# Optimization experiments

Hardware: AMD Instinct MI355X
Metric: run time of the kernel (lower is better)

## Reference

```python
import jax, jax.numpy as jnp
import numpy as np

B, C, IN_LEN, OUT_LEN, E, TOP_K, N_I = 1, 8192, 512, 512, 8, 2, 16


def setup_inputs() -> dict:
    key = jax.random.key(0)
    ks = jax.random.split(key, 8)
    w = lambda k, shape, sc=0.02: jax.random.normal(k, shape, dtype=jnp.float32) * sc
    return {
        "x": jax.random.normal(ks[0], (B, C, IN_LEN), dtype=jnp.float32),
        "Ins_tk": jax.random.normal(ks[1], (B, N_I, OUT_LEN), dtype=jnp.float32),
        "gate_w": w(ks[2], (IN_LEN, E)),            # Gate: Linear(in_len, E, bias=False)
        "expert_w": w(ks[3], (E, IN_LEN, OUT_LEN)),  # per-expert Linear weight (transposed)
        "expert_b": jnp.zeros((E, OUT_LEN), dtype=jnp.float32),
        "gamma_w": w(ks[4], (E, OUT_LEN)),          # EiLM gamma_generator: Linear(h,1,bias=False)
        "beta_w": w(ks[5], (E, OUT_LEN, OUT_LEN)),  # EiLM beta_generator (transposed)
        "rmod_w": w(ks[6], (OUT_LEN, E)),           # router_modulator: Linear(out_len, E, bias=False)
    }


def reference(x, Ins_tk, gate_w, expert_w, expert_b, gamma_w, beta_w, rmod_w):
    Bx, Cx, L = x.shape
    xf = x.reshape(-1, L)                                   # [N, in_len], N = B*C
    ins = Ins_tk[0]                                         # [N_i, out_len] (B==1 asserted)

    # Router: logits + expert-wise modulation of logits
    router_gamma = jnp.mean(ins @ rmod_w, axis=0)           # [E]
    logits = xf @ gate_w + router_gamma                     # [N, E]
    probs = jax.nn.softmax(logits.astype(jnp.float32), axis=-1)
    rw, sel = jax.lax.top_k(probs, TOP_K)                   # [N, k] values/indices (no renorm)

    # Combine weights per token per expert: sum_k rw[t,k] * onehot(sel[t,k])
    combine = jnp.sum(jax.nn.one_hot(sel, E, dtype=rw.dtype) * rw[..., None], axis=1)  # [N, E]

    # EiLM per-expert affine params: scalar gamma, vector beta (mean over instruction tokens)
    gam = jnp.mean(ins @ gamma_w.T, axis=0)                 # [E]
    bet = jnp.einsum('nh,ehd->ed', ins, beta_w) / N_I       # [E, out_len]

    # Per-expert linear over all tokens, then EiLM modulation
    eo = jnp.einsum('nl,eld->end', xf, expert_w) + expert_b[:, None, :]   # [E, N, out]
    mod = gam[:, None, None] * eo + bet[:, None, :]                        # [E, N, out]

    out = jnp.einsum('ne,end->nd', combine, mod)            # [N, out]
    return out.reshape(Bx, Cx, OUT_LEN)
```

## Files before the change

kernel.cpp:

```cpp
#include <hip/hip_runtime.h>
#include <hip/hip_bf16.h>

#define N_TOK 8192
#define INL   512
#define OUTL  512
#define NE    8
#define NI    16
#define EOFF  (OUTL * INL)

typedef unsigned short ushort_t;
typedef unsigned int   uint_t;
typedef short  short8  __attribute__((ext_vector_type(8)));
typedef float  floatx4 __attribute__((ext_vector_type(4)));

#define WS_CNT    0u
#define WS_GAM    4096u
#define WS_RGAM   4352u
#define WS_SCHED  4608u
#define WS_BET    8192u
#define WS_SELW   32768u
#define WS_WT     163840u
#define WS_LIST   4358144u
#define WS_XBF    6455296u
#define MAXTP     184

__device__ __forceinline__ ushort_t f2bf(float f) {
    uint_t b = __float_as_uint(f);
    return (ushort_t)((b + 0x7FFFu + ((b >> 16) & 1u)) >> 16);
}
__device__ __forceinline__ uint_t pkbf(float a, float b) {
    __hip_bfloat162 h = __float22bfloat162_rn(make_float2(a, b));
    union { __hip_bfloat162 h2; uint_t u; } cv;
    cv.h2 = h;
    return cv.u;
}
__device__ __forceinline__ void dma16(const ushort_t* g, ushort_t* l) {
    __builtin_amdgcn_global_load_lds(
        (const __attribute__((address_space(1))) void*)g,
        (__attribute__((address_space(3))) void*)l,
        16, 0, 0);
}

__global__ __launch_bounds__(256)
void k_prep(const float* __restrict__ x,
            const float* __restrict__ ins,
            const float* __restrict__ expert_w,
            const float* __restrict__ expert_b,
            const float* __restrict__ gamma_w,
            const float* __restrict__ beta_w,
            const float* __restrict__ rmod_w,
            ushort_t* __restrict__ wt,
            ushort_t* __restrict__ xbf,
            float* __restrict__ wsBet,
            float* __restrict__ wsGam, float* __restrict__ wsRgam,
            int* __restrict__ wsCnt) {
    __shared__ __align__(16) char smem[17152];
    int bx = blockIdx.x;
    int tid = threadIdx.x;

    if (bx < 512) {
        float (*tile)[65] = (float(*)[65])smem;
        int e = bx >> 6, rem = bx & 63;
        int lt = (rem >> 3) * 64, dt = (rem & 7) * 64;
        int dIdx = tid & 63, lq = tid >> 6;
        for (int i = 0; i < 16; ++i) {
            int l = lq * 16 + i;
            tile[l][dIdx] = expert_w[(e * INL + lt + l) * OUTL + dt + dIdx];
        }
        __syncthreads();
        int lIdx = tid & 63, dq = tid >> 6;
        for (int i = 0; i < 16; ++i) {
            int d = dq * 16 + i;
            wt[(e * OUTL + dt + d) * INL + lt + lIdx] = f2bf(tile[lIdx][d]);
        }
        return;
    }

    if (bx < 640) {
        float* sS  = (float*)smem;
        float* red = sS + 512;
        float* gamS = red + 256;
        int b2 = bx - 512;
        int e = b2 >> 4, dBase = (b2 & 15) * 32;
        for (int h = tid; h < INL; h += 256) {
            float a = 0.f;
            for (int n = 0; n < NI; ++n) a += ins[n * INL + h];
            sS[h] = a;
        }
        __syncthreads();
        if (tid < 64) {
            float g = 0.f;
            for (int j = 0; j < 8; ++j) g += sS[tid * 8 + j] * gamma_w[e * INL + tid * 8 + j];
            for (int off = 32; off >= 1; off >>= 1) g += __shfl_xor(g, off, 64);
            if (tid == 0) gamS[0] = g * (1.f / NI);
        }
        int doff = tid & 31, hq = tid >> 5;
        float a = 0.f;
        for (int j = 0; j < 64; ++j) {
            int h = hq * 64 + j;
            a += sS[h] * beta_w[(e * INL + h) * OUTL + dBase + doff];
        }
        red[tid] = a;
        __syncthreads();
        if (tid < 32) {
            float t = 0.f;
            for (int k = 0; k < 8; ++k) t += red[k * 32 + tid];
            int d = dBase + tid;
            wsBet[e * OUTL + d] = t * (1.f / NI) + gamS[0] * expert_b[e * OUTL + d];
        }
        return;
    }

    if (bx == 640) {
        if (tid < 64) wsCnt[tid * 16] = 0;
        float* sS = (float*)smem;
        float* pg = sS + 512;
        float* pr = pg + 64;
        for (int h = tid; h < INL; h += 256) {
            float a = 0.f;
            for (int n = 0; n < NI; ++n) a += ins[n * INL + h];
            sS[h] = a;
        }
        __syncthreads();
        if (tid < 64) {
            int e = tid & 7, qq = tid >> 3;
            float g = 0.f, r = 0.f;
            for (int j = 0; j < 64; ++j) {
                int h = qq * 64 + j;
                float sv = sS[h];
                g += sv * gamma_w[e * INL + h];
                r += sv * rmod_w[h * NE + e];
            }
            pg[tid] = g; pr[tid] = r;
        }
        __syncthreads();
        if (tid < NE) {
            float g = 0.f, r = 0.f;
            for (int qq = 0; qq < 8; ++qq) { g += pg[qq * 8 + tid]; r += pr[qq * 8 + tid]; }
            wsGam[tid]  = g * (1.f / NI);
            wsRgam[tid] = r * (1.f / NI);
        }
        return;
    }

    {
        int b2 = bx - 641;
        const float* xp = x + (size_t)b2 * 16384;
        ushort_t* xq = xbf + (size_t)b2 * 16384;
        #pragma unroll
        for (int j = 0; j < 16; ++j) {
            int o = j * 1024 + tid * 4;
            float4 v = *(const float4*)(xp + o);
            uint2 u;
            u.x = pkbf(v.x, v.y);
            u.y = pkbf(v.z, v.w);
            *(uint2*)(xq + o) = u;
        }
    }
}

__global__ __launch_bounds__(256)
void k_route(const float* __restrict__ x,
             const float* __restrict__ gate_w,
             const float* __restrict__ wsGam,
             const float* __restrict__ wsRgam,
             float4* __restrict__ selW,
             int* __restrict__ wsCnt, int* __restrict__ wsList) {
    __shared__ float gateT[NE * INL];
    __shared__ int tokP[16];
    __shared__ int cnt64[64], base64[64], pos[16];

    int tid = threadIdx.x;
    for (int i = 0; i < 16; ++i) {
        int f = tid + 256 * i;
        gateT[(f & 7) * INL + (f >> 3)] = gate_w[f];
    }
    if (tid < 64) cnt64[tid] = 0;
    __syncthreads();

    int w = tid >> 6, lane = tid & 63;
    int tbase = blockIdx.x * 16 + w * 4;

    for (int tt = 0; tt < 4; ++tt) {
        int t = tbase + tt;
        float2 xv[4];
        for (int i = 0; i < 4; ++i)
            xv[i] = *(const float2*)(x + (size_t)t * INL + 2 * lane + 128 * i);

        float acc[NE];
        for (int e = 0; e < NE; ++e) acc[e] = 0.f;
        for (int i = 0; i < 4; ++i) {
            int c = 2 * lane + 128 * i;
            for (int e = 0; e < NE; ++e)
                acc[e] += xv[i].x * gateT[e * INL + c] + xv[i].y * gateT[e * INL + c + 1];
        }
        for (int e = 0; e < NE; ++e) {
            float a = acc[e];
            for (int off = 32; off >= 1; off >>= 1) a += __shfl_xor(a, off, 64);
            acc[e] = a;
        }
        float logit[NE];
        for (int e = 0; e < NE; ++e) logit[e] = acc[e] + wsRgam[e];

        int i0 = 0; float m0 = logit[0];
        for (int e = 1; e < NE; ++e) if (logit[e] > m0) { m0 = logit[e]; i0 = e; }
        int i1 = -1; float m1 = -3.4e38f;
        for (int e = 0; e < NE; ++e) if (e != i0 && logit[e] > m1) { m1 = logit[e]; i1 = e; }

        float S = 0.f;
        for (int e = 0; e < NE; ++e) S += expf(logit[e] - m0);
        float rw0 = 1.0f / S;
        float rw1 = expf(m1 - m0) / S;

        if (lane == 0) {
            selW[t] = make_float4(rw0 * wsGam[i0], rw1 * wsGam[i1], rw0, rw1);
            tokP[w * 4 + tt] = i0 * 8 + i1;
        }
    }
    __syncthreads();

    if (tid < 16) pos[tid] = atomicAdd(&cnt64[tokP[tid]], 1);
    __syncthreads();
    if (tid < 64 && cnt64[tid] > 0)
        base64[tid] = atomicAdd(wsCnt + tid * 16, cnt64[tid]);
    __syncthreads();
    if (tid < 16) {
        int p = tokP[tid];
        wsList[(size_t)p * N_TOK + base64[p] + pos[tid]] = blockIdx.x * 16 + tid;
    }
}

__global__ __launch_bounds__(256)
void k_sched(const int* __restrict__ wsCnt, int* __restrict__ sched) {
    __shared__ int cnt[64], base[64], totS;
    int tid = threadIdx.x;
    if (tid < 64) cnt[tid] = wsCnt[tid * 16];
    __syncthreads();
    if (tid == 0) {
        int run = 0;
        for (int i = 0; i < 64; ++i) {
            base[i] = run;
            run += (cnt[i] + 63) >> 6;
        }
        totS = run;
    }
    __syncthreads();
    if (tid < 64) {
        int c = cnt[tid], ti = (c + 63) >> 6, b = base[tid];
        for (int j = 0; j < ti; ++j)
            sched[b + j] = tid | (j << 6) | (c << 14);
    }
    for (int j = totS + tid; j < MAXTP; j += 256)
        sched[j] = -1;
}

__global__ __launch_bounds__(256, 4)
void k_gemmp(const ushort_t* __restrict__ xbf, const ushort_t* __restrict__ wt,
             const int* __restrict__ sched, const int* __restrict__ wsList,
             const float4* __restrict__ selW, const float* __restrict__ wsBet,
             float* __restrict__ out) {
    int bx = blockIdx.x;
    int ct = bx / MAXTP;
    int bt = bx % MAXTP;

    int s = sched[bt];
    if (s < 0) return;
    int li = s & 63, lt = (s >> 6) & 127, cntE = s >> 14;
    int e0 = li >> 3, e1 = li & 7;
    const int* listE = wsList + (size_t)li * N_TOK;

    __shared__ ushort_t Blds[2][2][64 * 64];

    int tid = threadIdx.x;
    int wid = tid >> 6, lane = tid & 63;
    int wm = wid * 16;
    int mrow = lane & 15, laneq = lane >> 4, q8 = laneq * 8, qr = laneq * 4;

    int idx = lt * 64 + wm + mrow;
    int tok = 0;
    if (idx < cntE) tok = listE[idx];
    const ushort_t* arowp = xbf + (size_t)tok * INL + q8;

    int c0 = tid;
    int col0 = c0 >> 3, kg0 = ((c0 & 7) - col0) & 7;
    const ushort_t* pB = wt + (size_t)e0 * EOFF + (size_t)(ct * 64 + col0) * INL + kg0 * 8;
    ptrdiff_t dE = (ptrdiff_t)(e1 - e0) * EOFF;
    ushort_t* ldsA = &Blds[0][0][0] + wid * 512;

    int fcol[4], frot0[4];
    for (int nt = 0; nt < 4; ++nt) {
        fcol[nt] = nt * 16 + mrow;
        frot0[nt] = (laneq + fcol[nt]) & 7;
    }

    floatx4 acc[2][4];
    #pragma unroll
    for (int e = 0; e < 2; ++e)
        for (int nt = 0; nt < 4; ++nt) acc[e][nt] = (floatx4){0.f, 0.f, 0.f, 0.f};

    dma16(pB,                 ldsA);
    dma16(pB + 32 * INL,      ldsA + 2048);
    dma16(pB + dE,            ldsA + 4096);
    dma16(pB + dE + 32 * INL, ldsA + 6144);
    short8 ca0 = *(const short8*)(arowp);
    short8 ca1 = *(const short8*)(arowp + 32);
    __syncthreads();

    #pragma unroll
    for (int kc = 0; kc < 8; ++kc) {
        int buf = kc & 1;
        short8 na0, na1;
        if (kc < 7) {
            const ushort_t* p = pB + (kc + 1) * 64;
            ushort_t* l = ldsA + (buf ^ 1) * 8192;
            dma16(p,                 l);
            dma16(p + 32 * INL,      l + 2048);
            dma16(p + dE,            l + 4096);
            dma16(p + dE + 32 * INL, l + 6144);
            const ushort_t* ap = arowp + (kc + 1) * 64;
            na0 = *(const short8*)(ap);
            na1 = *(const short8*)(ap + 32);
        }

        const ushort_t* Bb = &Blds[buf][0][0];
        #pragma unroll
        for (int e = 0; e < 2; ++e) {
            const ushort_t* B = Bb + e * 4096;
            short8 bf[4][2];
            #pragma unroll
            for (int nt = 0; nt < 4; ++nt) {
                int cb = fcol[nt] * 64;
                bf[nt][0] = *(const short8*)&B[cb + frot0[nt] * 8];
                bf[nt][1] = *(const short8*)&B[cb + ((frot0[nt] + 4) & 7) * 8];
            }
            #pragma unroll
            for (int nt = 0; nt < 4; ++nt) {
                acc[e][nt] = __builtin_amdgcn_mfma_f32_16x16x32_bf16(
                    ca0, bf[nt][0], acc[e][nt], 0, 0, 0);
                acc[e][nt] = __builtin_amdgcn_mfma_f32_16x16x32_bf16(
                    ca1, bf[nt][1], acc[e][nt], 0, 0, 0);
            }
        }
        __syncthreads();
        if (kc < 7) { ca0 = na0; ca1 = na1; }
    }

    #pragma unroll
    for (int ri = 0; ri < 4; ++ri) {
        int idx2 = lt * 64 + wm + qr + ri;
        if (idx2 >= cntE) continue;
        int tok2 = listE[idx2];
        float4 w4 = selW[tok2];
        float* op = out + (size_t)tok2 * OUTL + ct * 64;
        #pragma unroll
        for (int nt = 0; nt < 4; ++nt) {
            int col = ct * 64 + nt * 16 + mrow;
            float bet = w4.z * wsBet[e0 * OUTL + col] + w4.w * wsBet[e1 * OUTL + col];
            op[nt * 16 + mrow] = w4.x * acc[0][nt][ri] + w4.y * acc[1][nt][ri] + bet;
        }
    }
}

extern "C" void kernel_launch(void* const* d_in, const int* in_sizes, int n_in,
                              void* d_out, int out_size, void* d_ws, size_t ws_size,
                              hipStream_t stream) {
    const float* x        = (const float*)d_in[0];
    const float* ins      = (const float*)d_in[1];
    const float* gate_w   = (const float*)d_in[2];
    const float* expert_w = (const float*)d_in[3];
    const float* expert_b = (const float*)d_in[4];
    const float* gamma_w  = (const float*)d_in[5];
    const float* beta_w   = (const float*)d_in[6];
    const float* rmod_w   = (const float*)d_in[7];
    float* out = (float*)d_out;

    char* ws = (char*)d_ws;
    int*      wsCnt  = (int*)(ws + WS_CNT);
    float*    wsGam  = (float*)(ws + WS_GAM);
    float*    wsRgam = (float*)(ws + WS_RGAM);
    int*      wsSch  = (int*)(ws + WS_SCHED);
    float*    wsBet  = (float*)(ws + WS_BET);
    float4*   selW   = (float4*)(ws + WS_SELW);
    ushort_t* wt     = (ushort_t*)(ws + WS_WT);
    int*      wsList = (int*)(ws + WS_LIST);
    ushort_t* xbf    = (ushort_t*)(ws + WS_XBF);

    k_prep<<<897, 256, 0, stream>>>(x, ins, expert_w, expert_b,
                                    gamma_w, beta_w, rmod_w,
                                    wt, xbf, wsBet, wsGam, wsRgam, wsCnt);
    k_route<<<N_TOK / 16, 256, 0, stream>>>(x, gate_w, wsGam, wsRgam,
                                            selW, wsCnt, wsList);
    k_sched<<<1, 256, 0, stream>>>(wsCnt, wsSch);
    k_gemmp<<<MAXTP * 8, 256, 0, stream>>>(xbf, wt, wsSch, wsList,
                                           selW, wsBet, out);
}
```

Measured before the change: 130.9 us.

## Fuse prep, routing and scheduling into one kernel; compute schedule inside GEMM

Merges the prep and routing kernels into one launch. Each routing block now recomputes the router gamma and EiLM gamma itself instead of reading them from a separate block. The single-thread scheduling kernel is removed: every GEMM block rebuilds its tile assignment from the pair counts with a wave-level prefix scan and ballot. The counter reset moves to a hipMemsetAsync. This cuts two kernel launches and their serial dependencies, at the cost of redundant gamma computation in 512 routing blocks and a small scan in every GEMM block.

```diff
diff --git a/kernel.cpp b/kernel.cpp
--- a/kernel.cpp
+++ b/kernel.cpp
@@ -14,9 +14,6 @@
 typedef float  floatx4 __attribute__((ext_vector_type(4)));
 
 #define WS_CNT    0u
-#define WS_GAM    4096u
-#define WS_RGAM   4352u
-#define WS_SCHED  4608u
 #define WS_BET    8192u
 #define WS_SELW   32768u
 #define WS_WT     163840u
@@ -42,19 +39,20 @@
 }
 
 __global__ __launch_bounds__(256)
-void k_prep(const float* __restrict__ x,
-            const float* __restrict__ ins,
-            const float* __restrict__ expert_w,
-            const float* __restrict__ expert_b,
-            const float* __restrict__ gamma_w,
-            const float* __restrict__ beta_w,
-            const float* __restrict__ rmod_w,
-            ushort_t* __restrict__ wt,
-            ushort_t* __restrict__ xbf,
-            float* __restrict__ wsBet,
-            float* __restrict__ wsGam, float* __restrict__ wsRgam,
-            int* __restrict__ wsCnt) {
-    __shared__ __align__(16) char smem[17152];
+void k_fused(const float* __restrict__ x,
+             const float* __restrict__ ins,
+             const float* __restrict__ expert_w,
+             const float* __restrict__ expert_b,
+             const float* __restrict__ gamma_w,
+             const float* __restrict__ beta_w,
+             const float* __restrict__ rmod_w,
+             const float* __restrict__ gate_w,
+             ushort_t* __restrict__ wt,
+             ushort_t* __restrict__ xbf,
+             float* __restrict__ wsBet,
+             float4* __restrict__ selW,
+             int* __restrict__ wsCnt, int* __restrict__ wsList) {
+    __shared__ __align__(16) char smem[20480];
     int bx = blockIdx.x;
     int tid = threadIdx.x;
 
@@ -111,40 +109,8 @@
         return;
     }
 
-    if (bx == 640) {
-        if (tid < 64) wsCnt[tid * 16] = 0;
-        float* sS = (float*)smem;
-        float* pg = sS + 512;
-        float* pr = pg + 64;
-        for (int h = tid; h < INL; h += 256) {
-            float a = 0.f;
-            for (int n = 0; n < NI; ++n) a += ins[n * INL + h];
-            sS[h] = a;
-        }
-        __syncthreads();
-        if (tid < 64) {
-            int e = tid & 7, qq = tid >> 3;
-            float g = 0.f, r = 0.f;
-            for (int j = 0; j < 64; ++j) {
-                int h = qq * 64 + j;
-                float sv = sS[h];
-                g += sv * gamma_w[e * INL + h];
-                r += sv * rmod_w[h * NE + e];
-            }
-            pg[tid] = g; pr[tid] = r;
-        }
-        __syncthreads();
-        if (tid < NE) {
-            float g = 0.f, r = 0.f;
-            for (int qq = 0; qq < 8; ++qq) { g += pg[qq * 8 + tid]; r += pr[qq * 8 + tid]; }
-            wsGam[tid]  = g * (1.f / NI);
-            wsRgam[tid] = r * (1.f / NI);
-        }
-        return;
-    }
-
-    {
-        int b2 = bx - 641;
+    if (bx < 896) {
+        int b2 = bx - 640;
         const float* xp = x + (size_t)b2 * 16384;
         ushort_t* xq = xbf + (size_t)b2 * 16384;
         #pragma unroll
@@ -156,114 +122,140 @@
             u.y = pkbf(v.z, v.w);
             *(uint2*)(xq + o) = u;
         }
-    }
-}
-
-__global__ __launch_bounds__(256)
-void k_route(const float* __restrict__ x,
-             const float* __restrict__ gate_w,
-             const float* __restrict__ wsGam,
-             const float* __restrict__ wsRgam,
-             float4* __restrict__ selW,
-             int* __restrict__ wsCnt, int* __restrict__ wsList) {
-    __shared__ float gateT[NE * INL];
-    __shared__ int tokP[16];
-    __shared__ int cnt64[64], base64[64], pos[16];
-
-    int tid = threadIdx.x;
-    for (int i = 0; i < 16; ++i) {
-        int f = tid + 256 * i;
-        gateT[(f & 7) * INL + (f >> 3)] = gate_w[f];
-    }
-    if (tid < 64) cnt64[tid] = 0;
-    __syncthreads();
-
-    int w = tid >> 6, lane = tid & 63;
-    int tbase = blockIdx.x * 16 + w * 4;
-
-    for (int tt = 0; tt < 4; ++tt) {
-        int t = tbase + tt;
-        float2 xv[4];
-        for (int i = 0; i < 4; ++i)
-            xv[i] = *(const float2*)(x + (size_t)t * INL + 2 * lane + 128 * i);
-
-        float acc[NE];
-        for (int e = 0; e < NE; ++e) acc[e] = 0.f;
-        for (int i = 0; i < 4; ++i) {
-            int c = 2 * lane + 128 * i;
-            for (int e = 0; e < NE; ++e)
-                acc[e] += xv[i].x * gateT[e * INL + c] + xv[i].y * gateT[e * INL + c + 1];
-        }
-        for (int e = 0; e < NE; ++e) {
-            float a = acc[e];
-            for (int off = 32; off >= 1; off >>= 1) a += __shfl_xor(a, off, 64);
-            acc[e] = a;
-        }
-        float logit[NE];
-        for (int e = 0; e < NE; ++e) logit[e] = acc[e] + wsRgam[e];
-
-        int i0 = 0; float m0 = logit[0];
-        for (int e = 1; e < NE; ++e) if (logit[e] > m0) { m0 = logit[e]; i0 = e; }
-        int i1 = -1; float m1 = -3.4e38f;
-        for (int e = 0; e < NE; ++e) if (e != i0 && logit[e] > m1) { m1 = logit[e]; i1 = e; }
-
-        float S = 0.f;
-        for (int e = 0; e < NE; ++e) S += expf(logit[e] - m0);
-        float rw0 = 1.0f / S;
-        float rw1 = expf(m1 - m0) / S;
-
-        if (lane == 0) {
-            selW[t] = make_float4(rw0 * wsGam[i0], rw1 * wsGam[i1], rw0, rw1);
-            tokP[w * 4 + tt] = i0 * 8 + i1;
-        }
-    }
-    __syncthreads();
-
-    if (tid < 16) pos[tid] = atomicAdd(&cnt64[tokP[tid]], 1);
-    __syncthreads();
-    if (tid < 64 && cnt64[tid] > 0)
-        base64[tid] = atomicAdd(wsCnt + tid * 16, cnt64[tid]);
-    __syncthreads();
-    if (tid < 16) {
-        int p = tokP[tid];
-        wsList[(size_t)p * N_TOK + base64[p] + pos[tid]] = blockIdx.x * 16 + tid;
-    }
-}
-
-__global__ __launch_bounds__(256)
-void k_sched(const int* __restrict__ wsCnt, int* __restrict__ sched) {
-    __shared__ int cnt[64], base[64], totS;
-    int tid = threadIdx.x;
-    if (tid < 64) cnt[tid] = wsCnt[tid * 16];
-    __syncthreads();
-    if (tid == 0) {
-        int run = 0;
-        for (int i = 0; i < 64; ++i) {
-            base[i] = run;
-            run += (cnt[i] + 63) >> 6;
-        }
-        totS = run;
-    }
-    __syncthreads();
-    if (tid < 64) {
-        int c = cnt[tid], ti = (c + 63) >> 6, b = base[tid];
-        for (int j = 0; j < ti; ++j)
-            sched[b + j] = tid | (j << 6) | (c << 14);
-    }
-    for (int j = totS + tid; j < MAXTP; j += 256)
-        sched[j] = -1;
+        return;
+    }
+
+    {
+        int rb = bx - 896;
+        float* sS   = (float*)smem;
+        float* pg   = sS + 512;
+        float* pr   = pg + 64;
+        float* gam8 = pr + 64;
+        float* rg8  = gam8 + 8;
+        int*   tokP  = (int*)(smem + 2624);
+        int*   cnt64 = tokP + 16;
+        int*   base64 = cnt64 + 64;
+        int*   pos   = base64 + 64;
+        float* gateT = (float*)(smem + 4096);
+
+        for (int h = tid; h < INL; h += 256) {
+            float a = 0.f;
+            for (int n = 0; n < NI; ++n) a += ins[n * INL + h];
+            sS[h] = a;
+        }
+        __syncthreads();
+        if (tid < 64) {
+            int e = tid & 7, qq = tid >> 3;
+            float g = 0.f, r = 0.f;
+            for (int j = 0; j < 64; ++j) {
+                int h = qq * 64 + j;
+                float sv = sS[h];
+                g += sv * gamma_w[e * INL + h];
+                r += sv * rmod_w[h * NE + e];
+            }
+            pg[tid] = g; pr[tid] = r;
+        }
+        __syncthreads();
+        if (tid < NE) {
+            float g = 0.f, r = 0.f;
+            for (int qq = 0; qq < 8; ++qq) { g += pg[qq * 8 + tid]; r += pr[qq * 8 + tid]; }
+            gam8[tid] = g * (1.f / NI);
+            rg8[tid]  = r * (1.f / NI);
+        }
+        for (int i = 0; i < 16; ++i) {
+            int f = tid + 256 * i;
+            gateT[(f & 7) * INL + (f >> 3)] = gate_w[f];
+        }
+        if (tid < 64) cnt64[tid] = 0;
+        __syncthreads();
+
+        int w = tid >> 6, lane = tid & 63;
+        int tbase = rb * 16 + w * 4;
+
+        for (int tt = 0; tt < 4; ++tt) {
+            int t = tbase + tt;
+            float2 xv[4];
+            for (int i = 0; i < 4; ++i)
+                xv[i] = *(const float2*)(x + (size_t)t * INL + 2 * lane + 128 * i);
+
+            float acc[NE];
+            for (int e = 0; e < NE; ++e) acc[e] = 0.f;
+            for (int i = 0; i < 4; ++i) {
+                int c = 2 * lane + 128 * i;
+                for (int e = 0; e < NE; ++e)
+                    acc[e] += xv[i].x * gateT[e * INL + c] + xv[i].y * gateT[e * INL + c + 1];
+            }
+            for (int e = 0; e < NE; ++e) {
+                float a = acc[e];
+                for (int off = 32; off >= 1; off >>= 1) a += __shfl_xor(a, off, 64);
+                acc[e] = a;
+            }
+            float logit[NE];
+            for (int e = 0; e < NE; ++e) logit[e] = acc[e] + rg8[e];
+
+            int i0 = 0; float m0 = logit[0];
+            for (int e = 1; e < NE; ++e) if (logit[e] > m0) { m0 = logit[e]; i0 = e; }
+            int i1 = -1; float m1 = -3.4e38f;
+            for (int e = 0; e < NE; ++e) if (e != i0 && logit[e] > m1) { m1 = logit[e]; i1 = e; }
+
+            float S = 0.f;
+            for (int e = 0; e < NE; ++e) S += expf(logit[e] - m0);
+            float rw0 = 1.0f / S;
+            float rw1 = expf(m1 - m0) / S;
+
+            if (lane == 0) {
+                selW[t] = make_float4(rw0 * gam8[i0], rw1 * gam8[i1], rw0, rw1);
+                tokP[w * 4 + tt] = i0 * 8 + i1;
+            }
+        }
+        __syncthreads();
+
+        if (tid < 16) pos[tid] = atomicAdd(&cnt64[tokP[tid]], 1);
+        __syncthreads();
+        if (tid < 64 && cnt64[tid] > 0)
+            base64[tid] = atomicAdd(wsCnt + tid * 16, cnt64[tid]);
+        __syncthreads();
+        if (tid < 16) {
+            int p = tokP[tid];
+            wsList[(size_t)p * N_TOK + base64[p] + pos[tid]] = rb * 16 + tid;
+        }
+    }
 }
 
 __global__ __launch_bounds__(256, 4)
 void k_gemmp(const ushort_t* __restrict__ xbf, const ushort_t* __restrict__ wt,
-             const int* __restrict__ sched, const int* __restrict__ wsList,
+             const int* __restrict__ wsCnt, const int* __restrict__ wsList,
              const float4* __restrict__ selW, const float* __restrict__ wsBet,
              float* __restrict__ out) {
     int bx = blockIdx.x;
     int ct = bx / MAXTP;
     int bt = bx % MAXTP;
-
-    int s = sched[bt];
+    int tid = threadIdx.x;
+
+    __shared__ int sWord;
+    if (tid < 64) {
+        int cnt = wsCnt[tid * 16];
+        int ti = (cnt + 63) >> 6;
+        int incl = ti;
+        #pragma unroll
+        for (int off = 1; off < 64; off <<= 1) {
+            int v = __shfl_up(incl, off, 64);
+            if ((tid & 63) >= off) incl += v;
+        }
+        int base = incl - ti;
+        int hit = (bt >= base) && (bt < incl);
+        unsigned long long m = __ballot(hit);
+        int word = -1;
+        if (m) {
+            int src = __ffsll((unsigned long long)m) - 1;
+            int b2 = __shfl(base, src, 64);
+            int c2 = __shfl(cnt, src, 64);
+            word = src | ((bt - b2) << 6) | (c2 << 14);
+        }
+        if (tid == 0) sWord = word;
+    }
+    __syncthreads();
+    int s = sWord;
     if (s < 0) return;
     int li = s & 63, lt = (s >> 6) & 127, cntE = s >> 14;
     int e0 = li >> 3, e1 = li & 7;
@@ -271,7 +263,6 @@
 
     __shared__ ushort_t Blds[2][2][64 * 64];
 
-    int tid = threadIdx.x;
     int wid = tid >> 6, lane = tid & 63;
     int wm = wid * 16;
     int mrow = lane & 15, laneq = lane >> 4, q8 = laneq * 8, qr = laneq * 4;
@@ -376,21 +367,16 @@
 
     char* ws = (char*)d_ws;
     int*      wsCnt  = (int*)(ws + WS_CNT);
-    float*    wsGam  = (float*)(ws + WS_GAM);
-    float*    wsRgam = (float*)(ws + WS_RGAM);
-    int*      wsSch  = (int*)(ws + WS_SCHED);
     float*    wsBet  = (float*)(ws + WS_BET);
     float4*   selW   = (float4*)(ws + WS_SELW);
     ushort_t* wt     = (ushort_t*)(ws + WS_WT);
     int*      wsList = (int*)(ws + WS_LIST);
     ushort_t* xbf    = (ushort_t*)(ws + WS_XBF);
 
-    k_prep<<<897, 256, 0, stream>>>(x, ins, expert_w, expert_b,
-                                    gamma_w, beta_w, rmod_w,
-                                    wt, xbf, wsBet, wsGam, wsRgam, wsCnt);
-    k_route<<<N_TOK / 16, 256, 0, stream>>>(x, gate_w, wsGam, wsRgam,
-                                            selW, wsCnt, wsList);
-    k_sched<<<1, 256, 0, stream>>>(wsCnt, wsSch);
-    k_gemmp<<<MAXTP * 8, 256, 0, stream>>>(xbf, wt, wsSch, wsList,
+    hipMemsetAsync(wsCnt, 0, 4096, stream);
+    k_fused<<<1408, 256, 0, stream>>>(x, ins, expert_w, expert_b,
+                                      gamma_w, beta_w, rmod_w, gate_w,
+                                      wt, xbf, wsBet, selW, wsCnt, wsList);
+    k_gemmp<<<MAXTP * 8, 256, 0, stream>>>(xbf, wt, wsCnt, wsList,
                                            selW, wsBet, out);
 }
```

Result: slower. 136.2 us (+4.0%).
